# Optimization experiments

Measured on AMD Instinct MI355X. Metric: run time of the kernel, lower is better.

## Reference

```python
import jax, jax.numpy as jnp
import numpy as np

N = 100000   # nodes per graph (protein == ligand node count, forced by cat dim=1)
E = 3200000  # edges per graph (avg degree 32)
F = 128      # input feature dim
A = 10       # action dim


def _fanin_uniform(key, shape, fanin=None):
    fanin = fanin or shape[0]
    v = 1.0 / np.sqrt(fanin)
    return jax.random.uniform(key, shape, jnp.float32, -v, v)


def setup_inputs() -> dict:
    key = jax.random.key(0)
    ks = jax.random.split(key, 24)
    inp = {
        "protein_x": jax.random.normal(ks[0], (N, F), jnp.float32),
        "protein_edges": jax.random.randint(ks[1], (2, E), 0, N, jnp.int32),
        "ligand_x": jax.random.normal(ks[2], (N, F), jnp.float32),
        "ligand_edges": jax.random.randint(ks[3], (2, E), 0, N, jnp.int32),
        "action": jax.random.normal(ks[4], (N, A), jnp.float32),
        # protein GraphConv layers
        "wp1s": _fanin_uniform(ks[5], (F, 16)),
        "wp1n": _fanin_uniform(ks[6], (F, 16)),
        "bp1": jnp.zeros((16,), jnp.float32),
        "wp2s": _fanin_uniform(ks[7], (16, 50)),
        "wp2n": _fanin_uniform(ks[8], (16, 50)),
        "bp2": jnp.zeros((50,), jnp.float32),
        # ligand GraphConv layers
        "wl1s": _fanin_uniform(ks[9], (F, 16)),
        "wl1n": _fanin_uniform(ks[10], (F, 16)),
        "bl1": jnp.zeros((16,), jnp.float32),
        "wl2s": _fanin_uniform(ks[11], (16, 50)),
        "wl2n": _fanin_uniform(ks[12], (16, 50)),
        "bl2": jnp.zeros((50,), jnp.float32),
        # MLP head
        "w_in": _fanin_uniform(ks[13], (100, 60)),
        "b_in": jnp.zeros((60,), jnp.float32),
        "w_hid": _fanin_uniform(ks[14], (60 + A, 10)),
        "b_hid": jnp.zeros((10,), jnp.float32),
        "w_out": jax.random.uniform(ks[15], (10, 1), jnp.float32, -0.003, 0.003),
        "b_out": jnp.zeros((1,), jnp.float32),
    }
    return inp


def graph_conv(x, edge_index, w_self, w_nbr, b):
    # PyG GraphConv: x_i' = x_i @ W_self + (sum_{j->i} x_j) @ W_nbr + b
    src, dst = edge_index[0], edge_index[1]
    agg = jax.ops.segment_sum(x[src], dst, num_segments=x.shape[0])  # [N, Fin]
    return x @ w_self + agg @ w_nbr + b


def reference(protein_x, protein_edges, ligand_x, ligand_edges, action,
              wp1s, wp1n, bp1, wp2s, wp2n, bp2,
              wl1s, wl1n, bl1, wl2s, wl2n, bl2,
              w_in, b_in, w_hid, b_hid, w_out, b_out):
    # protein branch (dropout is identity in eval mode)
    p = jax.nn.relu(graph_conv(protein_x, protein_edges, wp1s, wp1n, bp1))
    p = graph_conv(p, protein_edges, wp2s, wp2n, bp2)            # [N, 50]
    # ligand branch
    l = jax.nn.relu(graph_conv(ligand_x, ligand_edges, wl1s, wl1n, bl1))
    l = graph_conv(l, ligand_edges, wl2s, wl2n, bl2)             # [N, 50]
    molecule = jnp.concatenate([p, l], axis=1)                   # [N, 100]
    finger_print = jax.nn.relu(molecule @ w_in + b_in)           # [N, 60]
    policy = jnp.concatenate([finger_print, action], axis=1) @ w_hid + b_hid
    policy = jax.nn.relu(policy) @ w_out + b_out                 # [N, 1]
    return policy
```

## Files before the change

kernel.cpp:

```cpp
#include <hip/hip_runtime.h>
#include <hip/hip_bf16.h>
#include <stdint.h>


#define F_IN 128
#define NBMAX 512
#define BIN_CH 16
#define BIN_EDGES (256 * BIN_CH)
#define FINE_CAP 12288

#define OW1P  0
#define OB1P  4096
#define OW1L  4112
#define OB1L  8208
#define OC1P  8224
#define OC2P  9184
#define OC1L  10144
#define OC2L  11104
#define OBIN  12064
#define OWHID 12124
#define OBHID 12824
#define OWOUT 12834
#define OBOUT 12844
#define WBUF_FLOATS 16384

__device__ __forceinline__ float bf2f(unsigned short u) {
    union { unsigned int i; float f; } v; v.i = ((unsigned int)u) << 16; return v.f;
}
__device__ __forceinline__ float bflo(unsigned int u) {
    union { unsigned int i; float f; } v; v.i = u << 16; return v.f;
}
__device__ __forceinline__ float bfhi(unsigned int u) {
    union { unsigned int i; float f; } v; v.i = u & 0xffff0000u; return v.f;
}
__device__ __forceinline__ unsigned short f2bf(float f) {
    union { float f; unsigned int i; } v; v.f = f;
    unsigned int u = v.i;
    unsigned int r = (u + 0x7fffu + ((u >> 16) & 1u)) >> 16;
    return (unsigned short)r;
}
__device__ __forceinline__ unsigned pack2bf(float a, float b) {
    return (unsigned)f2bf(a) | ((unsigned)f2bf(b) << 16);
}
__device__ __forceinline__ float ldf(const void* p, int isf32, size_t i) {
    return isf32 ? ((const float*)p)[i] : bf2f(((const unsigned short*)p)[i]);
}


struct PW {
    const void *wp1s, *wp1n, *bp1, *wl1s, *wl1n, *bl1;
    const void *wp2s, *wp2n, *bp2, *wl2s, *wl2n, *bl2;
    const void *w_in, *b_in, *w_hid, *b_hid, *w_out, *b_out;
};

__global__ __launch_bounds__(256) void k_prepw(
    PW P, const unsigned short* __restrict__ px, float* __restrict__ wb,
    int* __restrict__ flag, int* __restrict__ zp, int zn)
{
    __shared__ int cnt_s;
    if (threadIdx.x == 0) cnt_s = 0;
    __syncthreads();
    int bad = 0;
    for (int i = threadIdx.x; i < 4096; i += 256) {
        unsigned e = (px[i] >> 7) & 0xFFu;
        if (e >= 140u) bad++;
    }
    atomicAdd(&cnt_s, bad);
    __syncthreads();
    const int isf32 = (cnt_s > 4096 / 16) ? 1 : 0;
    if (threadIdx.x == 0 && blockIdx.x == 0) *flag = isf32;

    int t = blockIdx.x * 256 + threadIdx.x;
    int stride = gridDim.x * 256;
    for (int i = t; i < zn; i += stride) zp[i] = 0;

    for (int i = t; i < 4096; i += stride) {
        int k = i >> 5, j = i & 31;
        wb[OW1P + i] = (j < 16) ? ldf(P.wp1s, isf32, k * 16 + j)
                                : ldf(P.wp1n, isf32, k * 16 + (j - 16));
        wb[OW1L + i] = (j < 16) ? ldf(P.wl1s, isf32, k * 16 + j)
                                : ldf(P.wl1n, isf32, k * 16 + (j - 16));
    }
    for (int i = t; i < 16; i += stride) {
        wb[OB1P + i] = ldf(P.bp1, isf32, i);
        wb[OB1L + i] = ldf(P.bl1, isf32, i);
    }
    for (int i = t; i < 960; i += stride) {
        int k = i / 60, j = i % 60;
        float s1 = 0.f, s2 = 0.f;
        for (int r = 0; r < 50; ++r) {
            float wi = ldf(P.w_in, isf32, r * 60 + j);
            s1 += ldf(P.wp2s, isf32, k * 50 + r) * wi;
            s2 += ldf(P.wp2n, isf32, k * 50 + r) * wi;
        }
        wb[OC1P + i] = s1; wb[OC2P + i] = s2;
    }
    for (int i = t; i < 960; i += stride) {
        int k = i / 60, j = i % 60;
        float s1 = 0.f, s2 = 0.f;
        for (int r = 0; r < 50; ++r) {
            float wi = ldf(P.w_in, isf32, (50 + r) * 60 + j);
            s1 += ldf(P.wl2s, isf32, k * 50 + r) * wi;
            s2 += ldf(P.wl2n, isf32, k * 50 + r) * wi;
        }
        wb[OC1L + i] = s1; wb[OC2L + i] = s2;
    }
    for (int i = t; i < 60; i += stride) {
        float s = ldf(P.b_in, isf32, i);
        for (int r = 0; r < 50; ++r) {
            s += ldf(P.bp2, isf32, r) * ldf(P.w_in, isf32, r * 60 + i);
            s += ldf(P.bl2, isf32, r) * ldf(P.w_in, isf32, (50 + r) * 60 + i);
        }
        wb[OBIN + i] = s;
    }
    for (int i = t; i < 700; i += stride) wb[OWHID + i] = ldf(P.w_hid, isf32, i);
    for (int i = t; i < 10; i += stride) {
        wb[OBHID + i] = ldf(P.b_hid, isf32, i);
        wb[OWOUT + i] = ldf(P.w_out, isf32, i);
    }
    if (t == 0) wb[OBOUT] = ldf(P.b_out, isf32, 0);
}


__global__ __launch_bounds__(256) void k_bucket_hist(
    const int* __restrict__ ed0, const int* __restrict__ ed1,
    int* __restrict__ cnt, int nE)
{
    const int* ed = blockIdx.y ? ed1 : ed0;
    int* c = cnt + blockIdx.y * NBMAX;
    __shared__ int h[NBMAX];
    for (int i = threadIdx.x; i < NBMAX; i += 256) h[i] = 0;
    __syncthreads();
    int stride = gridDim.x * 256;
    for (int e = blockIdx.x * 256 + threadIdx.x; e < nE; e += stride)
        atomicAdd(&h[ed[e] >> 8], 1);
    __syncthreads();
    for (int i = threadIdx.x; i < NBMAX; i += 256)
        if (h[i]) atomicAdd(&c[i], h[i]);
}

__global__ __launch_bounds__(512) void k_bucket_scan(
    const int* __restrict__ cnt, int* __restrict__ base,
    int* __restrict__ cursor, int nb)
{
    const int* c = cnt + blockIdx.x * NBMAX;
    int* ba = base + blockIdx.x * 528;
    int* cu = cursor + blockIdx.x * NBMAX;
    __shared__ int sh[512];
    int t = threadIdx.x;
    int v = (t < nb) ? c[t] : 0;
    sh[t] = v;
    __syncthreads();
    for (int off = 1; off < 512; off <<= 1) {
        int x = (t >= off) ? sh[t - off] : 0;
        __syncthreads();
        sh[t] += x;
        __syncthreads();
    }
    int excl = sh[t] - v;
    if (t < nb) { ba[t] = excl; cu[t] = excl; }
    if (t == nb - 1) ba[nb] = excl + v;
}

__global__ __launch_bounds__(256) void k_bucket_bin(
    const int* __restrict__ es0, const int* __restrict__ ed0,
    const int* __restrict__ es1, const int* __restrict__ ed1,
    int* __restrict__ cursor, unsigned* __restrict__ pairs, int nE)
{
    const int* es = blockIdx.y ? es1 : es0;
    const int* ed = blockIdx.y ? ed1 : ed0;
    int* cur = cursor + blockIdx.y * NBMAX;
    unsigned* pr = pairs + (size_t)blockIdx.y * nE;

    __shared__ int h[NBMAX];
    __shared__ int lcur[NBMAX];
    __shared__ int sh[256];
    __shared__ unsigned stage[BIN_EDGES];
    __shared__ unsigned short stageB[BIN_EDGES];

    for (int i = threadIdx.x; i < NBMAX; i += 256) h[i] = 0;
    __syncthreads();
    int e0 = blockIdx.x * BIN_EDGES;
    int s[BIN_CH], d[BIN_CH];
#pragma unroll
    for (int k = 0; k < BIN_CH; ++k) {
        int e = e0 + k * 256 + threadIdx.x;
        if (e < nE) {
            s[k] = es[e]; d[k] = ed[e];
            atomicAdd(&h[d[k] >> 8], 1);
        } else d[k] = -1;
    }
    __syncthreads();
    {
        int t = threadIdx.x;
        int a = h[2 * t], b2 = h[2 * t + 1];
        sh[t] = a + b2;
        __syncthreads();
        for (int off = 1; off < 256; off <<= 1) {
            int x = (t >= off) ? sh[t - off] : 0;
            __syncthreads();
            sh[t] += x;
            __syncthreads();
        }
        int excl = sh[t] - (a + b2);
        lcur[2 * t] = excl;
        lcur[2 * t + 1] = excl + a;
    }
    __syncthreads();
    for (int b = threadIdx.x; b < NBMAX; b += 256) {
        int c = h[b];
        if (c) {
            int g = atomicAdd(&cur[b], c);
            h[b] = g - lcur[b];
        }
    }
    __syncthreads();
#pragma unroll
    for (int k = 0; k < BIN_CH; ++k) {
        if (d[k] >= 0) {
            int b = d[k] >> 8;
            int pos = atomicAdd(&lcur[b], 1);
            stage[pos] = ((unsigned)(d[k] & 255) << 24) | (unsigned)s[k];
            stageB[pos] = (unsigned short)b;
        }
    }
    __syncthreads();
    int total = nE - e0; if (total > BIN_EDGES) total = BIN_EDGES;
    for (int i = threadIdx.x; i < total; i += 256)
        pr[h[stageB[i]] + i] = stage[i];
}

__global__ __launch_bounds__(256) void k_bucket_fine(
    const unsigned* __restrict__ pairs, const int* __restrict__ base,
    int* __restrict__ row0, int* __restrict__ srcs0,
    int* __restrict__ row1, int* __restrict__ srcs1,
    int n, int nE, int nb)
{
    const unsigned* pr = pairs + (size_t)blockIdx.y * nE;
    const int* ba = base + blockIdx.y * 528;
    int* row = blockIdx.y ? row1 : row0;
    int* srcs = blockIdx.y ? srcs1 : srcs0;
    __shared__ int cnt[256], cur[256];
    __shared__ int stage[FINE_CAP];
    int b = blockIdx.x;
    int t = threadIdx.x;
    int s0 = ba[b], s1 = ba[b + 1];
    int m = s1 - s0;
    cnt[t] = 0;
    __syncthreads();
    for (int i = s0 + t; i < s1; i += 256)
        atomicAdd(&cnt[pr[i] >> 24], 1);
    __syncthreads();
    int c = cnt[t];
    cur[t] = c;
    __syncthreads();
    for (int off = 1; off < 256; off <<= 1) {
        int x = (t >= off) ? cur[t - off] : 0;
        __syncthreads();
        cur[t] += x;
        __syncthreads();
    }
    int excl = cur[t] - c;
    __syncthreads();
    int node = (b << 8) + t;
    if (node < n) row[node] = s0 + excl;
    if (b == nb - 1 && t == 0) row[n] = nE;
    if (m <= FINE_CAP) {
        cur[t] = excl;
        __syncthreads();
        for (int i = s0 + t; i < s1; i += 256) {
            unsigned p = pr[i];
            int slot = atomicAdd(&cur[p >> 24], 1);
            stage[slot] = (int)(p & 0xFFFFFFu);
        }
        __syncthreads();
        for (int i = t; i < m; i += 256)
            srcs[s0 + i] = stage[i];
    } else {
        cur[t] = s0 + excl;
        __syncthreads();
        for (int i = s0 + t; i < s1; i += 256) {
            unsigned p = pr[i];
            int slot = atomicAdd(&cur[p >> 24], 1);
            srcs[slot] = (int)(p & 0xFFFFFFu);
        }
    }
}


struct TArgs2 {
    const void* __restrict__ x;
    const float* __restrict__ w;
    const float* __restrict__ b;
    float* __restrict__ acc;
    void* __restrict__ nbr;
};

__global__ __launch_bounds__(512) void k_transform1(
    TArgs2 a0, TArgs2 a1, int n, const int* __restrict__ flag)
{
    TArgs2 A = blockIdx.y ? a1 : a0;
    const int isf32 = *flag;
    __shared__ float xs[64 * 128];
    const int t = threadIdx.x;
    const int tile0 = blockIdx.x * 64;

    if (isf32) {
        const float4* xg = (const float4*)A.x;
        float4* xl = (float4*)xs;
#pragma unroll
        for (int i = 0; i < 4; ++i) {
            int flat = i * 512 + t;
            int row = flat >> 5, ck = flat & 31;
            if (tile0 + row < n)
                xl[row * 32 + (ck ^ (row & 7))] =
                    xg[((size_t)(tile0 + row)) * 32 + ck];
        }
    } else {
        const uint4* xg = (const uint4*)A.x;
        float4* xl = (float4*)xs;
#pragma unroll
        for (int i = 0; i < 2; ++i) {
            int flat = i * 512 + t;
            int row = flat >> 4, ck = flat & 15;
            if (tile0 + row < n) {
                uint4 q = xg[((size_t)(tile0 + row)) * 16 + ck];
                float4 lo = make_float4(bflo(q.x), bfhi(q.x), bflo(q.y), bfhi(q.y));
                float4 hi = make_float4(bflo(q.z), bfhi(q.z), bflo(q.w), bfhi(q.w));
                xl[row * 32 + ((2 * ck) ^ (row & 7))] = lo;
                xl[row * 32 + ((2 * ck + 1) ^ (row & 7))] = hi;
            }
        }
    }
    __syncthreads();

    const int jq = __builtin_amdgcn_readfirstlane(t >> 6);
    const int r = t & 63;
    const int node = tile0 + r;
    if (node >= n) return;
    const float* __restrict__ Wb = A.w + 4 * jq;
    const int sw = r & 7;

    float acc[4];
    if (jq < 4) {
#pragma unroll
        for (int j = 0; j < 4; ++j) acc[j] = A.b[4 * jq + j];
    } else {
#pragma unroll
        for (int j = 0; j < 4; ++j) acc[j] = 0.f;
    }

    const float4* xl = (const float4*)xs + r * 32;
    for (int kb = 0; kb < 4; ++kb) {
        float4 xq[8];
#pragma unroll
        for (int u = 0; u < 8; ++u)
            xq[u] = xl[(kb * 8 + u) ^ sw];
#pragma unroll
        for (int u = 0; u < 8; ++u) {
            int kk = kb * 8 + u;
            float xv[4] = {xq[u].x, xq[u].y, xq[u].z, xq[u].w};
#pragma unroll
            for (int h = 0; h < 4; ++h) {
                const float* __restrict__ w0 = Wb + (kk * 4 + h) * 32;
#pragma unroll
                for (int j = 0; j < 4; ++j) acc[j] += xv[h] * w0[j];
            }
        }
    }

    if (jq < 4) {
        float4* a4 = (float4*)(A.acc + (size_t)node * 16);
        a4[jq] = make_float4(acc[0], acc[1], acc[2], acc[3]);
    } else {
        unsigned short* nrow = (unsigned short*)A.nbr + ((size_t)node << 4)
                               + ((jq - 4) << 2);
        *(uint2*)nrow = make_uint2(pack2bf(acc[0], acc[1]),
                                   pack2bf(acc[2], acc[3]));
    }
}

struct GArgs { const int *row, *srcs; const void* val; float* out; void* rout; };

__global__ __launch_bounds__(256) void k_gather16(
    GArgs g0, GArgs g1, int n, int selfmode)
{
    GArgs G = (blockIdx.x & 1) ? g1 : g0;
    int t = (blockIdx.x >> 1) * 256 + threadIdx.x;
    int node = t >> 1;
    if (node >= n) return;
    int c = (t & 1) << 3;
    const unsigned short* vb = (const unsigned short*)G.val;
    int rs = G.row[node], re = G.row[node + 1];
    float4 sa = make_float4(0.f, 0.f, 0.f, 0.f);
    float4 sb = make_float4(0.f, 0.f, 0.f, 0.f);
    if (selfmode) {
        const float4* o4 = (const float4*)(G.out + ((size_t)node << 4) + c);
        sa = o4[0]; sb = o4[1];
    }
    int j = rs;
    for (; j + 16 <= re; j += 16) {
        int s[16];
        uint4 v[16];
#pragma unroll
        for (int u = 0; u < 16; ++u) s[u] = G.srcs[j + u];
#pragma unroll
        for (int u = 0; u < 16; ++u)
            v[u] = *(const uint4*)(vb + (((size_t)s[u]) << 4) + c);
#pragma unroll
        for (int u = 0; u < 16; ++u) {
            sa.x += bflo(v[u].x); sa.y += bfhi(v[u].x);
            sa.z += bflo(v[u].y); sa.w += bfhi(v[u].y);
            sb.x += bflo(v[u].z); sb.y += bfhi(v[u].z);
            sb.z += bflo(v[u].w); sb.w += bfhi(v[u].w);
        }
    }
    for (; j + 8 <= re; j += 8) {
        int s[8];
        uint4 v[8];
#pragma unroll
        for (int u = 0; u < 8; ++u) s[u] = G.srcs[j + u];
#pragma unroll
        for (int u = 0; u < 8; ++u)
            v[u] = *(const uint4*)(vb + (((size_t)s[u]) << 4) + c);
#pragma unroll
        for (int u = 0; u < 8; ++u) {
            sa.x += bflo(v[u].x); sa.y += bfhi(v[u].x);
            sa.z += bflo(v[u].y); sa.w += bfhi(v[u].y);
            sb.x += bflo(v[u].z); sb.y += bfhi(v[u].z);
            sb.z += bflo(v[u].w); sb.w += bfhi(v[u].w);
        }
    }
    for (; j < re; ++j) {
        uint4 v = *(const uint4*)(vb + (((size_t)G.srcs[j]) << 4) + c);
        sa.x += bflo(v.x); sa.y += bfhi(v.x);
        sa.z += bflo(v.y); sa.w += bfhi(v.y);
        sb.x += bflo(v.z); sb.y += bfhi(v.z);
        sb.z += bflo(v.w); sb.w += bfhi(v.w);
    }
    float4* o4 = (float4*)(G.out + ((size_t)node << 4) + c);
    o4[0] = sa; o4[1] = sb;
    if (selfmode) {
        unsigned short* orow = (unsigned short*)G.rout + ((size_t)node << 4) + c;
        *(uint4*)orow = make_uint4(
            pack2bf(fmaxf(sa.x, 0.f), fmaxf(sa.y, 0.f)),
            pack2bf(fmaxf(sa.z, 0.f), fmaxf(sa.w, 0.f)),
            pack2bf(fmaxf(sb.x, 0.f), fmaxf(sb.y, 0.f)),
            pack2bf(fmaxf(sb.z, 0.f), fmaxf(sb.w, 0.f)));
    }
}

__device__ __forceinline__ void fp_acc30(float* fp, const float* __restrict__ wb,
                                         int off, int jo,
                                         const float* __restrict__ row, bool dorelu)
{
    const float4* r4 = (const float4*)row;
    for (int kk = 0; kk < 4; ++kk) {
        float4 v = r4[kk];
        float xs[4] = {v.x, v.y, v.z, v.w};
        if (dorelu) {
            xs[0] = fmaxf(xs[0], 0.f); xs[1] = fmaxf(xs[1], 0.f);
            xs[2] = fmaxf(xs[2], 0.f); xs[3] = fmaxf(xs[3], 0.f);
        }
        const float* __restrict__ wq = wb + off + kk * 240 + jo;
#pragma unroll
        for (int h = 0; h < 4; ++h) {
#pragma unroll
            for (int j = 0; j < 30; ++j) fp[j] += xs[h] * wq[h * 60 + j];
        }
    }
}

__global__ __launch_bounds__(256) void k_headf(
    const float* __restrict__ hP, const float* __restrict__ gP,
    const float* __restrict__ hL, const float* __restrict__ gL,
    const void* __restrict__ action, const float* __restrict__ wb,
    void* __restrict__ out, int n, const int* __restrict__ flag)
{
    const int isf32 = *flag;
    __shared__ float hbuf[128][10];
    int w = threadIdx.x >> 6;
    int jh = __builtin_amdgcn_readfirstlane(w & 1);
    int slot = ((w >> 1) << 6) + (threadIdx.x & 63);
    int node = blockIdx.x * 128 + slot;
    int nodec = node < n ? node : (n - 1);
    const int jo = 30 * jh;

    float fp[30];
#pragma unroll
    for (int j = 0; j < 30; ++j) fp[j] = wb[OBIN + jo + j];

    fp_acc30(fp, wb, OC1P, jo, hP + (size_t)nodec * 16, true);
    fp_acc30(fp, wb, OC2P, jo, gP + (size_t)nodec * 16, false);
    fp_acc30(fp, wb, OC1L, jo, hL + (size_t)nodec * 16, true);
    fp_acc30(fp, wb, OC2L, jo, gL + (size_t)nodec * 16, false);

    float h[10];
#pragma unroll
    for (int j = 0; j < 10; ++j) h[j] = (jh == 0) ? wb[OBHID + j] : 0.f;
#pragma unroll
    for (int k = 0; k < 30; ++k) {
        float v = fmaxf(fp[k], 0.f);
#pragma unroll
        for (int j = 0; j < 10; ++j) h[j] += v * wb[OWHID + (jo + k) * 10 + j];
    }
    if (jh) {
#pragma unroll
        for (int j = 0; j < 10; ++j) hbuf[slot][j] = h[j];
    }
    __syncthreads();
    if (jh == 0) {
#pragma unroll
        for (int j = 0; j < 10; ++j) h[j] += hbuf[slot][j];
#pragma unroll
        for (int k = 0; k < 10; ++k) {
            float v = ldf(action, isf32, (size_t)nodec * 10 + k);
#pragma unroll
            for (int j = 0; j < 10; ++j) h[j] += v * wb[OWHID + (60 + k) * 10 + j];
        }
        float o = wb[OBOUT];
#pragma unroll
        for (int j = 0; j < 10; ++j) o += fmaxf(h[j], 0.f) * wb[OWOUT + j];
        if (node < n) {
            if (isf32) ((float*)out)[node] = o;
            else       ((unsigned short*)out)[node] = f2bf(o);
        }
    }
}

extern "C" void kernel_launch(void* const* d_in, const int* in_sizes, int n_in,
                              void* d_out, int out_size, void* d_ws, size_t ws_size,
                              hipStream_t stream)
{
    const void* px   = d_in[0];
    const int*  pe   = (const int*)d_in[1];
    const void* lx   = d_in[2];
    const int*  le   = (const int*)d_in[3];
    const void* act  = d_in[4];

    const int N = in_sizes[0] / F_IN;
    const int E = in_sizes[1] / 2;
    const int NB = (N + 255) >> 8;

    int* flag    = (int*)d_ws;
    int* cnt     = flag + 64;
    int* base    = cnt + 2 * NBMAX;
    int* cursorB = base + 2 * 528;
    float* wbuf  = (float*)(flag + 3200);
    int* rowP    = flag + 3200 + WBUF_FLOATS;
    int* srcsP   = rowP + (N + 64);
    int* rowL    = srcsP + E;
    int* srcsL   = rowL + (N + 64);
    float* dense = (float*)(srcsL + E);
    unsigned* pairs = (unsigned*)dense;

    float* accP = dense;
    float* accL = accP + (size_t)N * 16;
    float* aggP = accL + (size_t)N * 16;
    float* aggL = aggP + (size_t)N * 16;
    void*  n1P  = (void*)(aggL + (size_t)N * 16);
    void*  n1L  = (void*)((float*)n1P + (size_t)N * 8);
    void*  n2P  = (void*)((float*)n1L + (size_t)N * 8);
    void*  n2L  = (void*)((float*)n2P + (size_t)N * 8);

    const int nb64 = (N + 63) / 64;
    const int nb128 = (N + 127) / 128;
    const int gb2 = (N * 2 + 255) / 256;
    const int bb = (E + BIN_EDGES - 1) / BIN_EDGES;

    PW P{d_in[5], d_in[6], d_in[7], d_in[11], d_in[12], d_in[13],
         d_in[8], d_in[9], d_in[10], d_in[14], d_in[15], d_in[16],
         d_in[17], d_in[18], d_in[19], d_in[20], d_in[21], d_in[22]};
    k_prepw<<<32, 256, 0, stream>>>(P, (const unsigned short*)px, wbuf,
                                    flag, cnt, 2 * NBMAX);

    k_bucket_hist<<<dim3(512, 2), 256, 0, stream>>>(pe + E, le + E, cnt, E);
    k_bucket_scan<<<2, 512, 0, stream>>>(cnt, base, cursorB, NB);
    k_bucket_bin<<<dim3(bb, 2), 256, 0, stream>>>(pe, pe + E, le, le + E,
                                                  cursorB, pairs, E);
    k_bucket_fine<<<dim3(NB, 2), 256, 0, stream>>>(pairs, base, rowP, srcsP,
                                                   rowL, srcsL, N, E, NB);

    TArgs2 tP{px, wbuf + OW1P, wbuf + OB1P, accP, n1P};
    TArgs2 tL{lx, wbuf + OW1L, wbuf + OB1L, accL, n1L};
    k_transform1<<<dim3(nb64, 2), 512, 0, stream>>>(tP, tL, N, flag);

    GArgs g1P{rowP, srcsP, n1P, accP, n2P}, g1L{rowL, srcsL, n1L, accL, n2L};
    k_gather16<<<gb2 * 2, 256, 0, stream>>>(g1P, g1L, N, 1);

    GArgs g2P{rowP, srcsP, n2P, aggP, nullptr}, g2L{rowL, srcsL, n2L, aggL, nullptr};
    k_gather16<<<gb2 * 2, 256, 0, stream>>>(g2P, g2L, N, 0);

    k_headf<<<nb128, 256, 0, stream>>>(accP, aggP, accL, aggL, act, wbuf,
                                       d_out, N, flag);
}
```

Baseline: 473.4 us.

## Split gather edges across two lanes per node and widen fine bucketing blocks

After: 454.0 us. -4.1%, faster.

```diff
diff --git a/kernel.cpp b/kernel.cpp
--- a/kernel.cpp
+++ b/kernel.cpp
@@ -230,7 +230,7 @@
         pr[h[stageB[i]] + i] = stage[i];
 }
 
-__global__ __launch_bounds__(256) void k_bucket_fine(
+__global__ __launch_bounds__(512) void k_bucket_fine(
     const unsigned* __restrict__ pairs, const int* __restrict__ base,
     int* __restrict__ row0, int* __restrict__ srcs0,
     int* __restrict__ row1, int* __restrict__ srcs1,
@@ -246,40 +246,40 @@
     int t = threadIdx.x;
     int s0 = ba[b], s1 = ba[b + 1];
     int m = s1 - s0;
-    cnt[t] = 0;
-    __syncthreads();
-    for (int i = s0 + t; i < s1; i += 256)
+    if (t < 256) cnt[t] = 0;
+    __syncthreads();
+    for (int i = s0 + t; i < s1; i += 512)
         atomicAdd(&cnt[pr[i] >> 24], 1);
     __syncthreads();
-    int c = cnt[t];
-    cur[t] = c;
+    int c = (t < 256) ? cnt[t] : 0;
+    if (t < 256) cur[t] = c;
     __syncthreads();
     for (int off = 1; off < 256; off <<= 1) {
-        int x = (t >= off) ? cur[t - off] : 0;
-        __syncthreads();
-        cur[t] += x;
-        __syncthreads();
-    }
-    int excl = cur[t] - c;
+        int x = (t < 256 && t >= off) ? cur[t - off] : 0;
+        __syncthreads();
+        if (t < 256) cur[t] += x;
+        __syncthreads();
+    }
+    int excl = (t < 256) ? (cur[t] - c) : 0;
     __syncthreads();
     int node = (b << 8) + t;
-    if (node < n) row[node] = s0 + excl;
+    if (t < 256 && node < n) row[node] = s0 + excl;
     if (b == nb - 1 && t == 0) row[n] = nE;
     if (m <= FINE_CAP) {
-        cur[t] = excl;
-        __syncthreads();
-        for (int i = s0 + t; i < s1; i += 256) {
+        if (t < 256) cur[t] = excl;
+        __syncthreads();
+        for (int i = s0 + t; i < s1; i += 512) {
             unsigned p = pr[i];
             int slot = atomicAdd(&cur[p >> 24], 1);
             stage[slot] = (int)(p & 0xFFFFFFu);
         }
         __syncthreads();
-        for (int i = t; i < m; i += 256)
+        for (int i = t; i < m; i += 512)
             srcs[s0 + i] = stage[i];
     } else {
-        cur[t] = s0 + excl;
-        __syncthreads();
-        for (int i = s0 + t; i < s1; i += 256) {
+        if (t < 256) cur[t] = s0 + excl;
+        __syncthreads();
+        for (int i = s0 + t; i < s1; i += 512) {
             unsigned p = pr[i];
             int slot = atomicAdd(&cur[p >> 24], 1);
             srcs[slot] = (int)(p & 0xFFFFFFu);
@@ -387,19 +387,20 @@
 {
     GArgs G = (blockIdx.x & 1) ? g1 : g0;
     int t = (blockIdx.x >> 1) * 256 + threadIdx.x;
-    int node = t >> 1;
+    int node = t >> 2;
     if (node >= n) return;
-    int c = (t & 1) << 3;
+    const int q = t & 3;
+    const int e2 = q >> 1;
+    const int c = (q & 1) << 3;
     const unsigned short* vb = (const unsigned short*)G.val;
     int rs = G.row[node], re = G.row[node + 1];
+    int half = (re - rs + 1) >> 1;
+    int jb = e2 ? (rs + half) : rs;
+    int je = e2 ? re : (rs + half);
     float4 sa = make_float4(0.f, 0.f, 0.f, 0.f);
     float4 sb = make_float4(0.f, 0.f, 0.f, 0.f);
-    if (selfmode) {
-        const float4* o4 = (const float4*)(G.out + ((size_t)node << 4) + c);
-        sa = o4[0]; sb = o4[1];
-    }
-    int j = rs;
-    for (; j + 16 <= re; j += 16) {
+    int j = jb;
+    for (; j + 16 <= je; j += 16) {
         int s[16];
         uint4 v[16];
 #pragma unroll
@@ -415,7 +416,7 @@
             sb.z += bflo(v[u].w); sb.w += bfhi(v[u].w);
         }
     }
-    for (; j + 8 <= re; j += 8) {
+    for (; j + 8 <= je; j += 8) {
         int s[8];
         uint4 v[8];
 #pragma unroll
@@ -431,22 +432,33 @@
             sb.z += bflo(v[u].w); sb.w += bfhi(v[u].w);
         }
     }
-    for (; j < re; ++j) {
+    for (; j < je; ++j) {
         uint4 v = *(const uint4*)(vb + (((size_t)G.srcs[j]) << 4) + c);
         sa.x += bflo(v.x); sa.y += bfhi(v.x);
         sa.z += bflo(v.y); sa.w += bfhi(v.y);
         sb.x += bflo(v.z); sb.y += bfhi(v.z);
         sb.z += bflo(v.w); sb.w += bfhi(v.w);
     }
-    float4* o4 = (float4*)(G.out + ((size_t)node << 4) + c);
-    o4[0] = sa; o4[1] = sb;
-    if (selfmode) {
-        unsigned short* orow = (unsigned short*)G.rout + ((size_t)node << 4) + c;
-        *(uint4*)orow = make_uint4(
-            pack2bf(fmaxf(sa.x, 0.f), fmaxf(sa.y, 0.f)),
-            pack2bf(fmaxf(sa.z, 0.f), fmaxf(sa.w, 0.f)),
-            pack2bf(fmaxf(sb.x, 0.f), fmaxf(sb.y, 0.f)),
-            pack2bf(fmaxf(sb.z, 0.f), fmaxf(sb.w, 0.f)));
+    sa.x += __shfl_xor(sa.x, 2); sa.y += __shfl_xor(sa.y, 2);
+    sa.z += __shfl_xor(sa.z, 2); sa.w += __shfl_xor(sa.w, 2);
+    sb.x += __shfl_xor(sb.x, 2); sb.y += __shfl_xor(sb.y, 2);
+    sb.z += __shfl_xor(sb.z, 2); sb.w += __shfl_xor(sb.w, 2);
+    if (e2 == 0) {
+        float4* o4 = (float4*)(G.out + ((size_t)node << 4) + c);
+        if (selfmode) {
+            float4 pa = o4[0], pb = o4[1];
+            sa.x += pa.x; sa.y += pa.y; sa.z += pa.z; sa.w += pa.w;
+            sb.x += pb.x; sb.y += pb.y; sb.z += pb.z; sb.w += pb.w;
+        }
+        o4[0] = sa; o4[1] = sb;
+        if (selfmode) {
+            unsigned short* orow = (unsigned short*)G.rout + ((size_t)node << 4) + c;
+            *(uint4*)orow = make_uint4(
+                pack2bf(fmaxf(sa.x, 0.f), fmaxf(sa.y, 0.f)),
+                pack2bf(fmaxf(sa.z, 0.f), fmaxf(sa.w, 0.f)),
+                pack2bf(fmaxf(sb.x, 0.f), fmaxf(sb.y, 0.f)),
+                pack2bf(fmaxf(sb.z, 0.f), fmaxf(sb.w, 0.f)));
+        }
     }
 }
 
@@ -565,20 +577,20 @@
 
     const int nb64 = (N + 63) / 64;
     const int nb128 = (N + 127) / 128;
-    const int gb2 = (N * 2 + 255) / 256;
+    const int gb4 = (N * 4 + 255) / 256;
     const int bb = (E + BIN_EDGES - 1) / BIN_EDGES;
 
     PW P{d_in[5], d_in[6], d_in[7], d_in[11], d_in[12], d_in[13],
          d_in[8], d_in[9], d_in[10], d_in[14], d_in[15], d_in[16],
          d_in[17], d_in[18], d_in[19], d_in[20], d_in[21], d_in[22]};
-    k_prepw<<<32, 256, 0, stream>>>(P, (const unsigned short*)px, wbuf,
+    k_prepw<<<64, 256, 0, stream>>>(P, (const unsigned short*)px, wbuf,
                                     flag, cnt, 2 * NBMAX);
 
     k_bucket_hist<<<dim3(512, 2), 256, 0, stream>>>(pe + E, le + E, cnt, E);
     k_bucket_scan<<<2, 512, 0, stream>>>(cnt, base, cursorB, NB);
     k_bucket_bin<<<dim3(bb, 2), 256, 0, stream>>>(pe, pe + E, le, le + E,
                                                   cursorB, pairs, E);
-    k_bucket_fine<<<dim3(NB, 2), 256, 0, stream>>>(pairs, base, rowP, srcsP,
+    k_bucket_fine<<<dim3(NB, 2), 512, 0, stream>>>(pairs, base, rowP, srcsP,
                                                    rowL, srcsL, N, E, NB);
 
     TArgs2 tP{px, wbuf + OW1P, wbuf + OB1P, accP, n1P};
@@ -586,10 +598,10 @@
     k_transform1<<<dim3(nb64, 2), 512, 0, stream>>>(tP, tL, N, flag);
 
     GArgs g1P{rowP, srcsP, n1P, accP, n2P}, g1L{rowL, srcsL, n1L, accL, n2L};
-    k_gather16<<<gb2 * 2, 256, 0, stream>>>(g1P, g1L, N, 1);
+    k_gather16<<<gb4 * 2, 256, 0, stream>>>(g1P, g1L, N, 1);
 
     GArgs g2P{rowP, srcsP, n2P, aggP, nullptr}, g2L{rowL, srcsL, n2L, aggL, nullptr};
-    k_gather16<<<gb2 * 2, 256, 0, stream>>>(g2P, g2L, N, 0);
+    k_gather16<<<gb4 * 2, 256, 0, stream>>>(g2P, g2L, N, 0);
 
     k_headf<<<nb128, 256, 0, stream>>>(accP, aggP, accL, aggL, act, wbuf,
                                        d_out, N, flag);
```
